# Kernel optimization log

Hardware: AMD Instinct MI355X
Metric: run time of the kernel (lower is better)

The kernel has to match this reference:

```python
import jax, jax.numpy as jnp
import numpy as np

N_HEAD = 16
ROPE_BASE = 10000.0


def _rope(x, cos, sin):
    # x: [B,H,T,D]; cos/sin: [T,D/2] broadcast over B,H
    half = x.shape[-1] // 2
    x1, x2 = x[..., :half], x[..., half:]
    return jnp.concatenate([x1 * cos - x2 * sin, x1 * sin + x2 * cos], axis=-1)


def setup_inputs() -> dict:
    key = jax.random.key(0)
    k1, k2, k3 = jax.random.split(key, 3)
    C = 2048
    x = jax.random.normal(k1, (4, 2048, C), dtype=jnp.float32)
    w_qkv = jax.random.normal(k2, (C, 3 * C), dtype=jnp.float32) * 0.02
    w_proj = jax.random.normal(k3, (C, C), dtype=jnp.float32) * 0.02
    return {"x": x, "w_qkv": w_qkv, "w_proj": w_proj}


def reference(x, w_qkv, w_proj):
    B, T, C = x.shape
    H = N_HEAD
    D = C // H
    half = D // 2

    qkv = x @ w_qkv  # [B,T,3C]
    q, k, v = jnp.split(qkv, 3, axis=-1)
    # [B,T,C] -> [B,H,T,D]
    q = q.reshape(B, T, H, D).transpose(0, 2, 1, 3)
    k = k.reshape(B, T, H, D).transpose(0, 2, 1, 3)
    v = v.reshape(B, T, H, D).transpose(0, 2, 1, 3)

    # RoPE cache (start_pos = 0, no kv_cache / prefill path)
    inv_freq = 1.0 / (ROPE_BASE ** (jnp.arange(half, dtype=jnp.float32) / half))
    pos = jnp.arange(T, dtype=jnp.float32)
    freqs = pos[:, None] * inv_freq[None, :]  # [T, half]
    cos, sin = jnp.cos(freqs), jnp.sin(freqs)

    q = _rope(q, cos, sin)
    k = _rope(k, cos, sin)

    # scaled dot-product attention with explicit causal mask
    att = jnp.einsum("bhqd,bhkd->bhqk", q, k) / jnp.sqrt(jnp.asarray(D, x.dtype))
    causal = jnp.arange(T)[:, None] >= jnp.arange(T)[None, :]  # [T,T] bool
    att = jnp.where(causal, att, jnp.asarray(-jnp.inf, att.dtype))
    att = jax.nn.softmax(att, axis=-1)
    # dropout = identity (eval mode)
    out = jnp.einsum("bhqk,bhkd->bhqd", att, v)
    out = out.transpose(0, 2, 1, 3).reshape(B, T, C)
    out = out @ w_proj
    return out, k, v  # (output, new kv-cache)
```

## Files before the change

### kernel.cpp

```cpp
#include <hip/hip_runtime.h>
#include <math.h>

#define CDIM 2048
#define TDIM 2048
#define BDIM 4
#define HDIM 16
#define DDIM 128
#define M1   (BDIM * TDIM)
#define N1   (3 * CDIM)
#define KK   CDIM
#define NT   32

typedef unsigned short u16;
typedef __bf16 bf16x8 __attribute__((ext_vector_type(8)));
typedef float f32x4 __attribute__((ext_vector_type(4)));

__device__ __forceinline__ u16 f2b(float f) {
  union { float f; unsigned u; } x; x.f = f;
  unsigned r = x.u + 0x7fffu + ((x.u >> 16) & 1u);
  return (u16)(r >> 16);
}

__device__ __forceinline__ void gload_lds16(const void* g, void* l) {
  __builtin_amdgcn_global_load_lds(
      (__attribute__((address_space(1))) void*)g,
      (__attribute__((address_space(3))) void*)l, 16, 0, 0);
}

__global__ void convert_x(const float* __restrict__ x, u16* __restrict__ xb, int n4) {
  int i = blockIdx.x * blockDim.x + threadIdx.x;
  if (i < n4) {
    float4 v = ((const float4*)x)[i];
    unsigned long long o = (unsigned long long)f2b(v.x)
                         | ((unsigned long long)f2b(v.y) << 16)
                         | ((unsigned long long)f2b(v.z) << 32)
                         | ((unsigned long long)f2b(v.w) << 48);
    ((unsigned long long*)xb)[i] = o;
  }
}

__global__ void transpose_w(const float* __restrict__ w, u16* __restrict__ wt, int K, int N) {
  __shared__ float tile[32][33];
  const int n0 = blockIdx.x * 32, k0 = blockIdx.y * 32;
  const int tx = threadIdx.x & 31, ty = threadIdx.x >> 5;
  for (int r = ty; r < 32; r += 8)
    tile[r][tx] = w[(k0 + r) * N + n0 + tx];
  __syncthreads();
  for (int r = ty; r < 32; r += 8)
    wt[(n0 + r) * K + k0 + tx] = f2b(tile[tx][r]);
}

__global__ void rope_tab(float* __restrict__ cosT, float* __restrict__ sinT) {
  int i = blockIdx.x * blockDim.x + threadIdx.x;
  int t = i >> 6, d = i & 63;
  float inv = exp2f(-(float)d * (13.287712379549449f / 64.0f));
  float a = (float)t * inv;
  cosT[i] = cosf(a);
  sinT[i] = sinf(a);
}


#define VMW4 asm volatile("s_waitcnt vmcnt(4)" ::: "memory");
#define VMW2 asm volatile("s_waitcnt vmcnt(2)" ::: "memory");
#define VMW0 asm volatile("s_waitcnt vmcnt(0)" ::: "memory");
#define NOWAIT

#define GEMM256_TILE(bufA_, bufB_, nA_, nB_, kno_, STG, WMID, WEND)            \
  {                                                                            \
    __builtin_amdgcn_s_barrier();        \
    bf16x8 aX[4][2], aY[4][2], bX[2][2], bY[2][2];                             \
                                                     \
    _Pragma("unroll")                                                          \
    for (int i = 0; i < 4; ++i)                                                \
      _Pragma("unroll")                                                        \
      for (int kh = 0; kh < 2; ++kh)                                           \
        aX[i][kh] = *(const bf16x8*)&(bufA_)[aoff + i * 1024 +                 \
                                             (((kh * 4 + quad) ^ rsw) * 8)];   \
    _Pragma("unroll")                                                          \
    for (int j = 0; j < 2; ++j)                                                \
      _Pragma("unroll")                                                        \
      for (int kh = 0; kh < 2; ++kh)                                           \
        bX[j][kh] = *(const bf16x8*)&(bufB_)[boff + j * 1024 +                 \
                                             (((kh * 4 + quad) ^ rsw) * 8)];   \
                                                          \
    __builtin_amdgcn_s_setprio(1);                                             \
    _Pragma("unroll")                                                          \
    for (int i = 0; i < 4; ++i)                                                \
      _Pragma("unroll")                                                        \
      for (int j = 0; j < 2; ++j)                                              \
        _Pragma("unroll")                                                      \
        for (int kh = 0; kh < 2; ++kh)                                         \
          acc[i][j] = __builtin_amdgcn_mfma_f32_16x16x32_bf16(                 \
              aX[i][kh], bX[j][kh], acc[i][j], 0, 0, 0);                       \
    __builtin_amdgcn_s_setprio(0);                                             \
              \
    _Pragma("unroll")                                                          \
    for (int j = 0; j < 2; ++j)                                                \
      _Pragma("unroll")                                                        \
      for (int kh = 0; kh < 2; ++kh)                                           \
        bY[j][kh] = *(const bf16x8*)&(bufB_)[8192 + boff + j * 1024 +          \
                                             (((kh * 4 + quad) ^ rsw) * 8)];   \
    if (STG) {                                                                 \
      _Pragma("unroll")                                                        \
      for (int q = 0; q < 2; ++q)                                              \
        gload_lds16(AgBase + (q * 128) * KK + (kno_), &(nA_)[q * 4096 + ldsw]);\
      _Pragma("unroll")                                                        \
      for (int q = 0; q < 2; ++q)                                              \
        gload_lds16(BgBase + (q * 128) * KK + (kno_),                          \
                    &(nB_)[q * 4096 + ldsw]);                                  \
    }                                                                          \
    WMID                                                                       \
    __builtin_amdgcn_s_barrier();                       \
                                 \
    __builtin_amdgcn_s_setprio(1);                                             \
    _Pragma("unroll")                                                          \
    for (int i = 0; i < 4; ++i)                                                \
      _Pragma("unroll")                                                        \
      for (int j = 0; j < 2; ++j)                                              \
        _Pragma("unroll")                                                      \
        for (int kh = 0; kh < 2; ++kh)                                         \
          acc[i][2 + j] = __builtin_amdgcn_mfma_f32_16x16x32_bf16(             \
              aX[i][kh], bY[j][kh], acc[i][2 + j], 0, 0, 0);                   \
    __builtin_amdgcn_s_setprio(0);                                             \
             \
    _Pragma("unroll")                                                          \
    for (int i = 0; i < 4; ++i)                                                \
      _Pragma("unroll")                                                        \
      for (int kh = 0; kh < 2; ++kh)                                           \
        aY[i][kh] = *(const bf16x8*)&(bufA_)[8192 + aoff + i * 1024 +          \
                                             (((kh * 4 + quad) ^ rsw) * 8)];   \
    if (STG) {                                                                 \
      _Pragma("unroll")                                                        \
      for (int q = 0; q < 2; ++q)                                              \
        gload_lds16(BgBase + (q * 128 + 32) * KK + (kno_),                     \
                    &(nB_)[8192 + q * 4096 + ldsw]);                           \
    }                                                                          \
                                                          \
    __builtin_amdgcn_s_setprio(1);                                             \
    _Pragma("unroll")                                                          \
    for (int i = 0; i < 4; ++i)                                                \
      _Pragma("unroll")                                                        \
      for (int j = 0; j < 2; ++j)                                              \
        _Pragma("unroll")                                                      \
        for (int kh = 0; kh < 2; ++kh)                                         \
          acc[4 + i][2 + j] = __builtin_amdgcn_mfma_f32_16x16x32_bf16(         \
              aY[i][kh], bY[j][kh], acc[4 + i][2 + j], 0, 0, 0);               \
    __builtin_amdgcn_s_setprio(0);                                             \
    if (STG) {                                                                 \
      _Pragma("unroll")                                                        \
      for (int q = 0; q < 2; ++q)                                              \
        gload_lds16(AgBase + (q * 128 + 64) * KK + (kno_),                     \
                    &(nA_)[8192 + q * 4096 + ldsw]);                           \
    }                                                                          \
                    \
    __builtin_amdgcn_s_setprio(1);                                             \
    _Pragma("unroll")                                                          \
    for (int i = 0; i < 4; ++i)                                                \
      _Pragma("unroll")                                                        \
      for (int j = 0; j < 2; ++j)                                              \
        _Pragma("unroll")                                                      \
        for (int kh = 0; kh < 2; ++kh)                                         \
          acc[4 + i][j] = __builtin_amdgcn_mfma_f32_16x16x32_bf16(             \
              aY[i][kh], bX[j][kh], acc[4 + i][j], 0, 0, 0);                   \
    __builtin_amdgcn_s_setprio(0);                                             \
    WEND                                                                       \
  }

#define GEMM256_MAINLOOP(APTR, BPTR)                                           \
  const int rA = lane >> 3, cA = lane & 7;                                     \
  const int w8r = wave * 8 + rA;                                               \
  const int swz8 = (cA ^ rA) * 8;                                              \
  const u16* AgBase = (APTR) + (m0 + w8r) * KK + swz8;                         \
  const int nb = ((w8r >> 5) * 64) + (w8r & 31);                               \
  const u16* BgBase = (BPTR) + (n0 + nb) * KK + swz8;                          \
  const int ldsw = wave * 512;                                                 \
  const int rsw = c16 & 7;                                                     \
  const int aoff = (((wave >> 2) * 64) + c16) * 64;                            \
  const int boff = (((wave & 3) * 32) + c16) * 64;                             \
  f32x4 acc[8][4];                                                             \
  {                                                                            \
    f32x4 z = {0.f, 0.f, 0.f, 0.f};                                            \
    _Pragma("unroll")                                                          \
    for (int i = 0; i < 8; ++i)                                                \
      _Pragma("unroll")                                                        \
      for (int j = 0; j < 4; ++j) acc[i][j] = z;                               \
  }                                                                            \
     \
  _Pragma("unroll")                                                            \
  for (int q = 0; q < 2; ++q)                                                  \
    gload_lds16(AgBase + (q * 128) * KK, &lds[q * 4096 + ldsw]);               \
  _Pragma("unroll")                                                            \
  for (int q = 0; q < 2; ++q)                                                  \
    gload_lds16(BgBase + (q * 128) * KK, &lds[32768 + q * 4096 + ldsw]);       \
  _Pragma("unroll")                                                            \
  for (int q = 0; q < 2; ++q)                                                  \
    gload_lds16(BgBase + (q * 128 + 32) * KK,                                  \
                &lds[32768 + 8192 + q * 4096 + ldsw]);                         \
  _Pragma("unroll")                                                            \
  for (int q = 0; q < 2; ++q)                                                  \
    gload_lds16(AgBase + (q * 128 + 64) * KK, &lds[8192 + q * 4096 + ldsw]);   \
  VMW2                                                                         \
  for (int kt = 0; kt < NT - 1; ++kt) {                                        \
    const int cur = kt & 1;                                                    \
    const u16* bA = &lds[cur * 16384];                                         \
    const u16* bB = &lds[32768 + cur * 16384];                                 \
    u16* nA = &lds[(cur ^ 1) * 16384];                                         \
    u16* nB = &lds[32768 + (cur ^ 1) * 16384];                                 \
    const int kno = (kt + 1) * 64;                                             \
    GEMM256_TILE(bA, bB, nA, nB, kno, 1, VMW4, VMW2)                           \
  }                                                                            \
           \
  GEMM256_TILE((&lds[16384]), (&lds[32768 + 16384]), (&lds[0]),                \
               (&lds[32768]), 0, 0, VMW0, NOWAIT)

__global__ __launch_bounds__(512, 1) void gemm_qkv(
    const u16* __restrict__ A,
    const u16* __restrict__ Bt,
    const float* __restrict__ cosT, const float* __restrict__ sinT,
    u16* __restrict__ qb, u16* __restrict__ kb,
    float* __restrict__ kout, float* __restrict__ vout,
    u16* __restrict__ vtout)
{
  extern __shared__ __align__(16) u16 lds[];
  const int tid = threadIdx.x, wave = tid >> 6, lane = tid & 63;
  const int quad = lane >> 4, c16 = lane & 15;
  const int bid = blockIdx.y * 24 + blockIdx.x;
  const int swz = (bid & 7) * 96 + (bid >> 3);
  const int m0 = (swz / 24) * 256, n0 = (swz % 24) * 256;

  GEMM256_MAINLOOP(A, Bt)

  float* cbuf = (float*)lds;
  const int mat = n0 >> 11;
  const int hbase = (n0 & 2047) >> 7;
  const float qscale = 0.1275178689414753f;
#pragma unroll
  for (int pass = 0; pass < 4; ++pass) {
    __syncthreads();
    if ((wave >> 2) == (pass >> 1)) {
#pragma unroll
      for (int i = 0; i < 4; ++i) {
        const int mf = (pass & 1) * 4 + i;
#pragma unroll
        for (int j = 0; j < 4; ++j)
#pragma unroll
          for (int r = 0; r < 4; ++r)
            cbuf[(i * 16 + quad * 4 + r) * 261 + (wave & 3) * 64 + j * 16 + c16] = acc[mf][j][r];
      }
    }
    __syncthreads();
#pragma unroll
    for (int it = 0; it < 16; ++it) {
      int p = it * 512 + tid;
      int lr = p >> 7;
      int hc = (p >> 6) & 1;
      int d = p & 63;
      float x1 = cbuf[lr * 261 + hc * 128 + d];
      float x2 = cbuf[lr * 261 + hc * 128 + 64 + d];
      int mg = m0 + pass * 64 + lr;
      int b = mg >> 11, t = mg & 2047;
      int h = hbase + hc;
      int idx = ((b * HDIM + h) * TDIM + t) * DDIM + d;
      if (mat == 2) {
        vout[idx] = x1; vout[idx + 64] = x2;
      } else {
        float cs = cosT[t * 64 + d], sn = sinT[t * 64 + d];
        float o1 = x1 * cs - x2 * sn;
        float o2 = x1 * sn + x2 * cs;
        if (mat == 0) {
          qb[idx] = f2b(o1 * qscale); qb[idx + 64] = f2b(o2 * qscale);
        } else {
          kout[idx] = o1; kout[idx + 64] = o2;
          kb[idx] = f2b(o1); kb[idx + 64] = f2b(o2);
        }
      }
    }
    if (mat == 2) {
#pragma unroll
      for (int it = 0; it < 16; ++it) {
        int p = it * 512 + tid;
        int tl = p & 63;
        int c2 = p >> 6;
        float xA = cbuf[tl * 261 + c2];
        float xB = cbuf[tl * 261 + 128 + c2];
        int mg = m0 + pass * 64 + tl;
        int b = mg >> 11, t = mg & 2047;
        vtout[((b * HDIM + hbase) * DDIM + c2) * TDIM + t] = f2b(xA);
        vtout[((b * HDIM + hbase + 1) * DDIM + c2) * TDIM + t] = f2b(xB);
      }
    }
  }
}

__global__ __launch_bounds__(512, 1) void gemm_proj(
    const u16* __restrict__ A,
    const u16* __restrict__ Bt,
    float* __restrict__ out)
{
  extern __shared__ __align__(16) u16 lds[];
  const int tid = threadIdx.x, wave = tid >> 6, lane = tid & 63;
  const int quad = lane >> 4, c16 = lane & 15;
  const int bid = blockIdx.y * 8 + blockIdx.x;
  const int swz = (bid & 7) * 32 + (bid >> 3);
  const int m0 = (swz >> 3) * 256, n0 = (swz & 7) * 256;

  GEMM256_MAINLOOP(A, Bt)

  const int wm = (wave >> 2) * 128, wn = (wave & 3) * 64;
#pragma unroll
  for (int mf = 0; mf < 8; ++mf)
#pragma unroll
    for (int nf = 0; nf < 4; ++nf)
#pragma unroll
      for (int r = 0; r < 4; ++r)
        out[(m0 + wm + mf * 16 + quad * 4 + r) * CDIM + n0 + wn + nf * 16 + c16] =
            acc[mf][nf][r];
}

__global__ __launch_bounds__(256, 2) void attn(
    const u16* __restrict__ qb, const u16* __restrict__ kb,
    const u16* __restrict__ vt, u16* __restrict__ att)
{
  extern __shared__ __align__(16) u16 sh[];
  u16* const psm = sh + 32768;

  const int tid = threadIdx.x, wave = tid >> 6, lane = tid & 63;
  const int quad = lane >> 4, c16 = lane & 15;
  const int bx = blockIdx.x;
  const int bh = blockIdx.y;

  for (int hv = 0; hv < 2; ++hv) {
    const int qt = hv ? (7 - bx) : (bx + 8);
    const int q0 = qt * 128;

    {
      const u16* qg = qb + (bh * TDIM + q0) * DDIM;
      const int rowl = wave * 4 + (lane >> 4);
      const int ch = lane & 15;
#pragma unroll
      for (int r = 0; r < 8; ++r) {
        int row = r * 16 + rowl;
        gload_lds16(qg + row * DDIM + (ch ^ (row & 15)) * 8,
                    &sh[(r * 16 + wave * 4) * 128]);
      }
    }
    __syncthreads();
    bf16x8 qf[2][4];
#pragma unroll
    for (int g = 0; g < 2; ++g)
#pragma unroll
      for (int kp = 0; kp < 4; ++kp)
        qf[g][kp] = *(const bf16x8*)&sh[(g * 64 + wave * 16 + c16) * 128 +
                                        (((kp * 4 + quad) ^ c16) * 8)];
    __syncthreads();

    f32x4 o[2][8];
    f32x4 zero = {0.f, 0.f, 0.f, 0.f};
#pragma unroll
    for (int g = 0; g < 2; ++g)
#pragma unroll
      for (int jd = 0; jd < 8; ++jd) o[g][jd] = zero;
    float lrow[2][4];
#pragma unroll
    for (int g = 0; g < 2; ++g)
#pragma unroll
      for (int r = 0; r < 4; ++r) lrow[g][r] = 0.f;

    const int nchunk = 2 * qt + 2;

    const int rowl = wave * 4 + (lane >> 4);
    const int ch = lane & 15;
    const int rowv = wave * 8 + (lane >> 3);
    const int chv = lane & 7;
#define STAGE_KV(kcs, bufbase)                                                 \
    {                                                                          \
      const int kcs0 = (kcs) * 64;                                             \
      const u16* kg = kb + (bh * TDIM + kcs0) * DDIM;                          \
      _Pragma("unroll")                                                        \
      for (int r = 0; r < 4; ++r) {                                            \
        int row = r * 16 + rowl;                                               \
        gload_lds16(kg + row * DDIM + (ch ^ (row & 15)) * 8,                   \
                    &sh[(bufbase) + (r * 16 + wave * 4) * 128]);               \
      }                                                                        \
      const u16* vg = vt + bh * (DDIM * TDIM) + kcs0;                          \
      _Pragma("unroll")                                                        \
      for (int r = 0; r < 4; ++r) {                                            \
        int row = r * 32 + rowv;                                               \
        gload_lds16(vg + row * TDIM + (chv ^ (row & 7)) * 8,                   \
                    &sh[(bufbase) + 8192 + (r * 32 + wave * 8) * 64]);         \
      }                                                                        \
    }

    STAGE_KV(0, 0)

    for (int kc = 0; kc < nchunk; ++kc) {
      const int kc0 = kc * 64;
      const int cur = kc & 1;
      const u16* ksm = sh + cur * 16384;
      const u16* vsm = ksm + 8192;

      if (kc + 1 < nchunk) {
        STAGE_KV(kc + 1, (cur ^ 1) * 16384)
        asm volatile("s_waitcnt vmcnt(8)" ::: "memory");
      } else {
        asm volatile("s_waitcnt vmcnt(0)" ::: "memory");
      }
      asm volatile("s_barrier" ::: "memory");

      f32x4 st[2][4];
#pragma unroll
      for (int g = 0; g < 2; ++g)
#pragma unroll
        for (int j = 0; j < 4; ++j) st[g][j] = zero;
#pragma unroll
      for (int kp = 0; kp < 4; ++kp) {
#pragma unroll
        for (int j = 0; j < 4; ++j) {
          bf16x8 bk = *(const bf16x8*)&ksm[(j * 16 + c16) * 128 +
                                           (((kp * 4 + quad) ^ c16) * 8)];
          st[0][j] = __builtin_amdgcn_mfma_f32_16x16x32_bf16(qf[0][kp], bk, st[0][j], 0, 0, 0);
          st[1][j] = __builtin_amdgcn_mfma_f32_16x16x32_bf16(qf[1][kp], bk, st[1][j], 0, 0, 0);
        }
      }

      u16* const pw = psm + wave * 2048;
#pragma unroll
      for (int g = 0; g < 2; ++g) {
        const bool dg = (kc >= 2 * qt + g);
        const int qrow_base = q0 + g * 64 + wave * 16 + quad * 4;
#pragma unroll
        for (int r = 0; r < 4; ++r) {
          const int row16 = quad * 4 + r;
          float sum = 0.f;
#pragma unroll
          for (int j = 0; j < 4; ++j) {
            float sv = st[g][j][r];
            if (dg && (kc0 + j * 16 + c16 > qrow_base + r)) sv = -INFINITY;
            float p = exp2f(sv - 8.0f);
            sum += p;
            int chunk = (j * 2 + (c16 >> 3)) ^ (row16 & 7);
            pw[g * 1024 + row16 * 64 + chunk * 8 + (c16 & 7)] = f2b(p);
          }
          lrow[g][r] += sum;
        }
      }

      asm volatile("s_waitcnt lgkmcnt(0)" ::: "memory");

#pragma unroll
      for (int s = 0; s < 2; ++s) {
        const int chp = ((s * 4 + quad) ^ (c16 & 7)) * 8;
        bf16x8 ap0 = *(const bf16x8*)&pw[c16 * 64 + chp];
        bf16x8 ap1 = *(const bf16x8*)&pw[1024 + c16 * 64 + chp];
#pragma unroll
        for (int jd = 0; jd < 8; ++jd) {
          bf16x8 bv = *(const bf16x8*)&vsm[(jd * 16 + c16) * 64 + chp];
          o[0][jd] = __builtin_amdgcn_mfma_f32_16x16x32_bf16(ap0, bv, o[0][jd], 0, 0, 0);
          o[1][jd] = __builtin_amdgcn_mfma_f32_16x16x32_bf16(ap1, bv, o[1][jd], 0, 0, 0);
        }
      }
      asm volatile("s_barrier" ::: "memory");
    }
#undef STAGE_KV

    const int b = bh >> 4, h = bh & 15;
#pragma unroll
    for (int g = 0; g < 2; ++g) {
      float ri[4];
#pragma unroll
      for (int r = 0; r < 4; ++r) {
        float s = lrow[g][r];
        s += __shfl_xor(s, 1, 64);
        s += __shfl_xor(s, 2, 64);
        s += __shfl_xor(s, 4, 64);
        s += __shfl_xor(s, 8, 64);
        ri[r] = 1.f / s;
      }
#pragma unroll
      for (int jd = 0; jd < 8; ++jd)
#pragma unroll
        for (int r = 0; r < 4; ++r) {
          int t = q0 + g * 64 + wave * 16 + quad * 4 + r;
          att[(b * TDIM + t) * CDIM + h * DDIM + jd * 16 + c16] = f2b(o[g][jd][r] * ri[r]);
        }
    }
    __syncthreads();
  }
}

extern "C" void kernel_launch(void* const* d_in, const int* in_sizes, int n_in,
                              void* d_out, int out_size, void* d_ws, size_t ws_size,
                              hipStream_t stream) {
  (void)in_sizes; (void)n_in; (void)out_size; (void)ws_size;
  const float* x      = (const float*)d_in[0];
  const float* w_qkv  = (const float*)d_in[1];
  const float* w_proj = (const float*)d_in[2];
  float* out  = (float*)d_out;
  float* kout = out + 16777216;
  float* vout = out + 2 * 16777216;

  char* ws = (char*)d_ws;
  u16*   xb     = (u16*)(ws);
  u16*   wqkvT  = (u16*)(ws + 33554432);
  u16*   wprojT = (u16*)(ws + 58720256);
  float* cosT   = (float*)(ws + 67108864);
  float* sinT   = (float*)(ws + 67633152);
  u16*   qb     = (u16*)(ws + 68157440);
  u16*   kb     = (u16*)(ws + 101711872);
  u16*   vt     = (u16*)(ws + 135266304);
  u16*   att    = xb;

  static int attr_set = 0;
  if (!attr_set) {
    hipFuncSetAttribute((const void*)gemm_qkv,
                        hipFuncAttributeMaxDynamicSharedMemorySize, 131072);
    hipFuncSetAttribute((const void*)gemm_proj,
                        hipFuncAttributeMaxDynamicSharedMemorySize, 131072);
    hipFuncSetAttribute((const void*)attn,
                        hipFuncAttributeMaxDynamicSharedMemorySize, 81920);
    attr_set = 1;
  }

  convert_x<<<16384, 256, 0, stream>>>(x, xb, 4194304);
  transpose_w<<<dim3(192, 64), 256, 0, stream>>>(w_qkv, wqkvT, KK, N1);
  transpose_w<<<dim3(64, 64), 256, 0, stream>>>(w_proj, wprojT, KK, CDIM);
  rope_tab<<<512, 256, 0, stream>>>(cosT, sinT);
  gemm_qkv<<<dim3(24, 32), 512, 131072, stream>>>(xb, wqkvT, cosT, sinT, qb, kb, kout, vout, vt);
  attn<<<dim3(8, 64), 256, 81920, stream>>>(qb, kb, vt, att);
  gemm_proj<<<dim3(8, 32), 512, 131072, stream>>>(att, wprojT, out);
}
```

Measured before the change: 698.5 us.

## Split attention block across 8 waves, one 16-row query group per wave

The attention kernel now launches 512 threads per block instead of 256. Each wave owns 16 query rows instead of 32, which halves per-wave accumulators and register pressure, and the K/V staging loads are split across twice as many threads. The causal-mask condition is recomputed per wave. Shared memory per block is unchanged at 80 KB, so LDS may cap resident blocks per CU below the launch bound of 4. Each K/V chunk read from LDS now feeds half as many MFMAs per load, which lowers reuse.

New measurement: 689.1 us. No clear change (-1.3%).

```diff
diff --git a/kernel.cpp b/kernel.cpp
--- a/kernel.cpp
+++ b/kernel.cpp
@@ -317,7 +317,7 @@
             acc[mf][nf][r];
 }
 
-__global__ __launch_bounds__(256, 2) void attn(
+__global__ __launch_bounds__(512, 4) void attn(
     const u16* __restrict__ qb, const u16* __restrict__ kb,
     const u16* __restrict__ vt, u16* __restrict__ att)
 {
@@ -329,65 +329,56 @@
   const int bx = blockIdx.x;
   const int bh = blockIdx.y;
 
+  const int rlK = wave * 4 + (lane >> 4), chK = lane & 15;
+  const int rlV = wave * 8 + (lane >> 3), chV = lane & 7;
+
   for (int hv = 0; hv < 2; ++hv) {
     const int qt = hv ? (7 - bx) : (bx + 8);
     const int q0 = qt * 128;
 
     {
       const u16* qg = qb + (bh * TDIM + q0) * DDIM;
-      const int rowl = wave * 4 + (lane >> 4);
-      const int ch = lane & 15;
-#pragma unroll
-      for (int r = 0; r < 8; ++r) {
-        int row = r * 16 + rowl;
-        gload_lds16(qg + row * DDIM + (ch ^ (row & 15)) * 8,
-                    &sh[(r * 16 + wave * 4) * 128]);
+#pragma unroll
+      for (int r = 0; r < 4; ++r) {
+        int row = r * 32 + rlK;
+        gload_lds16(qg + row * DDIM + (chK ^ (row & 15)) * 8,
+                    &sh[(r * 32 + wave * 4) * 128]);
       }
     }
     __syncthreads();
-    bf16x8 qf[2][4];
-#pragma unroll
-    for (int g = 0; g < 2; ++g)
-#pragma unroll
-      for (int kp = 0; kp < 4; ++kp)
-        qf[g][kp] = *(const bf16x8*)&sh[(g * 64 + wave * 16 + c16) * 128 +
-                                        (((kp * 4 + quad) ^ c16) * 8)];
+    bf16x8 qf[4];
+#pragma unroll
+    for (int kp = 0; kp < 4; ++kp)
+      qf[kp] = *(const bf16x8*)&sh[(wave * 16 + c16) * 128 +
+                                   (((kp * 4 + quad) ^ c16) * 8)];
     __syncthreads();
 
-    f32x4 o[2][8];
+    f32x4 o[8];
     f32x4 zero = {0.f, 0.f, 0.f, 0.f};
 #pragma unroll
-    for (int g = 0; g < 2; ++g)
-#pragma unroll
-      for (int jd = 0; jd < 8; ++jd) o[g][jd] = zero;
-    float lrow[2][4];
-#pragma unroll
-    for (int g = 0; g < 2; ++g)
-#pragma unroll
-      for (int r = 0; r < 4; ++r) lrow[g][r] = 0.f;
+    for (int jd = 0; jd < 8; ++jd) o[jd] = zero;
+    float lrow[4];
+#pragma unroll
+    for (int r = 0; r < 4; ++r) lrow[r] = 0.f;
 
     const int nchunk = 2 * qt + 2;
 
-    const int rowl = wave * 4 + (lane >> 4);
-    const int ch = lane & 15;
-    const int rowv = wave * 8 + (lane >> 3);
-    const int chv = lane & 7;
 #define STAGE_KV(kcs, bufbase)                                                 \
     {                                                                          \
       const int kcs0 = (kcs) * 64;                                             \
       const u16* kg = kb + (bh * TDIM + kcs0) * DDIM;                          \
       _Pragma("unroll")                                                        \
-      for (int r = 0; r < 4; ++r) {                                            \
-        int row = r * 16 + rowl;                                               \
-        gload_lds16(kg + row * DDIM + (ch ^ (row & 15)) * 8,                   \
-                    &sh[(bufbase) + (r * 16 + wave * 4) * 128]);               \
+      for (int r = 0; r < 2; ++r) {                                            \
+        int row = r * 32 + rlK;                                                \
+        gload_lds16(kg + row * DDIM + (chK ^ (row & 15)) * 8,                  \
+                    &sh[(bufbase) + (r * 32 + wave * 4) * 128]);               \
       }                                                                        \
       const u16* vg = vt + bh * (DDIM * TDIM) + kcs0;                          \
       _Pragma("unroll")                                                        \
-      for (int r = 0; r < 4; ++r) {                                            \
-        int row = r * 32 + rowv;                                               \
-        gload_lds16(vg + row * TDIM + (chv ^ (row & 7)) * 8,                   \
-                    &sh[(bufbase) + 8192 + (r * 32 + wave * 8) * 64]);         \
+      for (int r = 0; r < 2; ++r) {                                            \
+        int row = r * 64 + rlV;                                                \
+        gload_lds16(vg + row * TDIM + (chV ^ (row & 7)) * 8,                   \
+                    &sh[(bufbase) + 8192 + (r * 64 + wave * 8) * 64]);         \
       }                                                                        \
     }
 
@@ -401,48 +392,42 @@
 
       if (kc + 1 < nchunk) {
         STAGE_KV(kc + 1, (cur ^ 1) * 16384)
-        asm volatile("s_waitcnt vmcnt(8)" ::: "memory");
+        asm volatile("s_waitcnt vmcnt(4)" ::: "memory");
       } else {
         asm volatile("s_waitcnt vmcnt(0)" ::: "memory");
       }
       asm volatile("s_barrier" ::: "memory");
 
-      f32x4 st[2][4];
-#pragma unroll
-      for (int g = 0; g < 2; ++g)
-#pragma unroll
-        for (int j = 0; j < 4; ++j) st[g][j] = zero;
+      f32x4 st[4];
+#pragma unroll
+      for (int j = 0; j < 4; ++j) st[j] = zero;
 #pragma unroll
       for (int kp = 0; kp < 4; ++kp) {
 #pragma unroll
         for (int j = 0; j < 4; ++j) {
           bf16x8 bk = *(const bf16x8*)&ksm[(j * 16 + c16) * 128 +
                                            (((kp * 4 + quad) ^ c16) * 8)];
-          st[0][j] = __builtin_amdgcn_mfma_f32_16x16x32_bf16(qf[0][kp], bk, st[0][j], 0, 0, 0);
-          st[1][j] = __builtin_amdgcn_mfma_f32_16x16x32_bf16(qf[1][kp], bk, st[1][j], 0, 0, 0);
+          st[j] = __builtin_amdgcn_mfma_f32_16x16x32_bf16(qf[kp], bk, st[j], 0, 0, 0);
         }
       }
 
-      u16* const pw = psm + wave * 2048;
-#pragma unroll
-      for (int g = 0; g < 2; ++g) {
-        const bool dg = (kc >= 2 * qt + g);
-        const int qrow_base = q0 + g * 64 + wave * 16 + quad * 4;
-#pragma unroll
-        for (int r = 0; r < 4; ++r) {
-          const int row16 = quad * 4 + r;
-          float sum = 0.f;
-#pragma unroll
-          for (int j = 0; j < 4; ++j) {
-            float sv = st[g][j][r];
-            if (dg && (kc0 + j * 16 + c16 > qrow_base + r)) sv = -INFINITY;
-            float p = exp2f(sv - 8.0f);
-            sum += p;
-            int chunk = (j * 2 + (c16 >> 3)) ^ (row16 & 7);
-            pw[g * 1024 + row16 * 64 + chunk * 8 + (c16 & 7)] = f2b(p);
-          }
-          lrow[g][r] += sum;
+      u16* const pw = psm + wave * 1024;
+      const bool dg = (kc0 + 63 > q0 + wave * 16);
+      const int qrow_base = q0 + wave * 16 + quad * 4;
+#pragma unroll
+      for (int r = 0; r < 4; ++r) {
+        const int row16 = quad * 4 + r;
+        float sum = 0.f;
+#pragma unroll
+        for (int j = 0; j < 4; ++j) {
+          float sv = st[j][r];
+          if (dg && (kc0 + j * 16 + c16 > qrow_base + r)) sv = -INFINITY;
+          float p = exp2f(sv - 8.0f);
+          sum += p;
+          int chunk = (j * 2 + (c16 >> 3)) ^ (row16 & 7);
+          pw[row16 * 64 + chunk * 8 + (c16 & 7)] = f2b(p);
         }
+        lrow[r] += sum;
       }
 
       asm volatile("s_waitcnt lgkmcnt(0)" ::: "memory");
@@ -450,13 +435,11 @@
 #pragma unroll
       for (int s = 0; s < 2; ++s) {
         const int chp = ((s * 4 + quad) ^ (c16 & 7)) * 8;
-        bf16x8 ap0 = *(const bf16x8*)&pw[c16 * 64 + chp];
-        bf16x8 ap1 = *(const bf16x8*)&pw[1024 + c16 * 64 + chp];
+        bf16x8 ap = *(const bf16x8*)&pw[c16 * 64 + chp];
 #pragma unroll
         for (int jd = 0; jd < 8; ++jd) {
           bf16x8 bv = *(const bf16x8*)&vsm[(jd * 16 + c16) * 64 + chp];
-          o[0][jd] = __builtin_amdgcn_mfma_f32_16x16x32_bf16(ap0, bv, o[0][jd], 0, 0, 0);
-          o[1][jd] = __builtin_amdgcn_mfma_f32_16x16x32_bf16(ap1, bv, o[1][jd], 0, 0, 0);
+          o[jd] = __builtin_amdgcn_mfma_f32_16x16x32_bf16(ap, bv, o[jd], 0, 0, 0);
         }
       }
       asm volatile("s_barrier" ::: "memory");
@@ -464,26 +447,23 @@
 #undef STAGE_KV
 
     const int b = bh >> 4, h = bh & 15;
-#pragma unroll
-    for (int g = 0; g < 2; ++g) {
-      float ri[4];
+    float ri[4];
+#pragma unroll
+    for (int r = 0; r < 4; ++r) {
+      float s = lrow[r];
+      s += __shfl_xor(s, 1, 64);
+      s += __shfl_xor(s, 2, 64);
+      s += __shfl_xor(s, 4, 64);
+      s += __shfl_xor(s, 8, 64);
+      ri[r] = 1.f / s;
+    }
+#pragma unroll
+    for (int jd = 0; jd < 8; ++jd)
 #pragma unroll
       for (int r = 0; r < 4; ++r) {
-        float s = lrow[g][r];
-        s += __shfl_xor(s, 1, 64);
-        s += __shfl_xor(s, 2, 64);
-        s += __shfl_xor(s, 4, 64);
-        s += __shfl_xor(s, 8, 64);
-        ri[r] = 1.f / s;
-      }
-#pragma unroll
-      for (int jd = 0; jd < 8; ++jd)
-#pragma unroll
-        for (int r = 0; r < 4; ++r) {
-          int t = q0 + g * 64 + wave * 16 + quad * 4 + r;
-          att[(b * TDIM + t) * CDIM + h * DDIM + jd * 16 + c16] = f2b(o[g][jd][r] * ri[r]);
-        }
-    }
+        int t = q0 + wave * 16 + quad * 4 + r;
+        att[(b * TDIM + t) * CDIM + h * DDIM + jd * 16 + c16] = f2b(o[jd][r] * ri[r]);
+      }
     __syncthreads();
   }
 }
@@ -526,6 +506,6 @@
   transpose_w<<<dim3(64, 64), 256, 0, stream>>>(w_proj, wprojT, KK, CDIM);
   rope_tab<<<512, 256, 0, stream>>>(cosT, sinT);
   gemm_qkv<<<dim3(24, 32), 512, 131072, stream>>>(xb, wqkvT, cosT, sinT, qb, kb, kout, vout, vt);
-  attn<<<dim3(8, 64), 256, 81920, stream>>>(qb, kb, vt, att);
+  attn<<<dim3(8, 64), 512, 81920, stream>>>(qb, kb, vt, att);
   gemm_proj<<<dim3(8, 32), 512, 131072, stream>>>(att, wprojT, out);
 }
```
